# Performance work log

Measured on AMD Instinct MI355X. Metric: run time of the kernel, lower is better.

The kernel has to match this reference:

```python
import jax, jax.numpy as jnp
import numpy as np

N_QUBITS = 8

# Quantum circuit math: starting from |0...0>, apply RX(x_i) then RY(theta_i) on each
# wire independently (product state preserved). Exact PauliZ expectation per wire:
#   RX(x)|0> = cos(x/2)|0> - i sin(x/2)|1>;  after RY(t):
#   <Z> = cos(x) * cos(t)
# This is the exact closed form of the full state-vector simulation the torch module runs.

def setup_inputs() -> dict:
    key = jax.random.key(0)
    k1, k2, k3, k4 = jax.random.split(key, 4)
    B, S, D, F = 4, 4096, 1024, 4096
    x = jax.random.normal(k1, (B, S, D), dtype=jnp.float32)
    theta = jax.random.normal(k2, (N_QUBITS,), dtype=jnp.float32)
    W1 = jax.random.normal(k3, (F, N_QUBITS), dtype=jnp.float32) * (1.0 / np.sqrt(N_QUBITS))
    W2 = jax.random.normal(k4, (D, F), dtype=jnp.float32) * (1.0 / np.sqrt(F))
    return {"x": x, "theta": theta, "W1": W1, "W2": W2}


def reference(x, theta, W1, W2):
    # Encoder only reads the first n_qubits features of each token.
    z = jnp.cos(x[..., :N_QUBITS]) * jnp.cos(theta)          # [B, S, Q] PauliZ expectations
    h = jax.nn.relu(jnp.einsum('bsq,fq->bsf', z, W1))        # [B, S, ffn_dim]
    return jnp.einsum('bsf,df->bsd', h, W2)                  # [B, S, embed_dim]
```

## Files before the change

### kernel.cpp

```cpp
#include <hip/hip_runtime.h>
#include <hip/hip_bf16.h>
#include <math.h>


using f32x4  = __attribute__((ext_vector_type(4))) float;
using bf16x8 = __attribute__((ext_vector_type(8))) short;
using i32x4  = __attribute__((ext_vector_type(4))) int;

#define M_TOT 16384
#define N_TOT 1024
#define K_TOT 4096
#define NKT   128
#define TILEB 16384

static const size_t H_BYTES   = (size_t)M_TOT * K_TOT * 2;
static const size_t W2B_BYTES = (size_t)N_TOT * K_TOT * 2;
static const size_t WS_NEED   = H_BYTES + W2B_BYTES;

#define SWZ32(row, bytecol) ((bytecol) ^ ((((row) >> 1) & 3) << 4))

#define GLD16(gp, lp) __builtin_amdgcn_global_load_lds( \
    (const __attribute__((address_space(1))) unsigned int*)(const void*)(gp), \
    (__attribute__((address_space(3))) unsigned int*)(void*)(lp), 16, 0, 0)

static __device__ inline unsigned short f2bf(float f) {
    __hip_bfloat16 b = __float2bfloat16(f);
    unsigned short u;
    __builtin_memcpy(&u, &b, 2);
    return u;
}

__global__ __launch_bounds__(256)
void k_h(const float* __restrict__ x, const float* __restrict__ theta,
         const float* __restrict__ W1, char* __restrict__ hws)
{
    __shared__ float sZ[256 * 8];
    __shared__ float sW[128 * 8];
    const int tid = threadIdx.x;
    const int bx  = blockIdx.x;
    const int by  = blockIdx.y;

    {
        const float* xp = x + ((size_t)bx * 256 + tid) * 1024;
        f32x4 a = *reinterpret_cast<const f32x4*>(xp);
        f32x4 b = *reinterpret_cast<const f32x4*>(xp + 4);
        #pragma unroll
        for (int q = 0; q < 4; ++q) {
            sZ[tid * 8 + q]     = cosf(a[q]) * cosf(theta[q]);
            sZ[tid * 8 + 4 + q] = cosf(b[q]) * cosf(theta[q + 4]);
        }
    }
    *reinterpret_cast<f32x4*>(&sW[tid * 4]) =
        *reinterpret_cast<const f32x4*>(W1 + (size_t)by * 1024 + tid * 4);
    __syncthreads();

    const int tm = tid >> 4;
    const int tk = tid & 15;

    f32x4 wA[8], wB[8];
    #pragma unroll
    for (int kk = 0; kk < 8; ++kk) {
        wA[kk] = *reinterpret_cast<const f32x4*>(&sW[(tk * 8 + kk) * 8]);
        wB[kk] = *reinterpret_cast<const f32x4*>(&sW[(tk * 8 + kk) * 8 + 4]);
    }

    const int kt    = by * 4 + (tk >> 2);
    const int slotb = (tk & 3) * 16;
    char* tb = hws + ((size_t)bx * NKT + kt) * TILEB;

    #pragma unroll
    for (int i = 0; i < 16; ++i) {
        const int row = tm * 16 + i;
        f32x4 za = *reinterpret_cast<const f32x4*>(&sZ[row * 8]);
        f32x4 zb = *reinterpret_cast<const f32x4*>(&sZ[row * 8 + 4]);
        unsigned hu[8];
        #pragma unroll
        for (int kk = 0; kk < 8; ++kk) {
            float h = 0.f;
            #pragma unroll
            for (int q = 0; q < 4; ++q) {
                h = fmaf(za[q], wA[kk][q], h);
                h = fmaf(zb[q], wB[kk][q], h);
            }
            hu[kk] = (unsigned)f2bf(fmaxf(h, 0.f));
        }
        i32x4 pk;
        pk[0] = (int)(hu[0] | (hu[1] << 16));
        pk[1] = (int)(hu[2] | (hu[3] << 16));
        pk[2] = (int)(hu[4] | (hu[5] << 16));
        pk[3] = (int)(hu[6] | (hu[7] << 16));
        *reinterpret_cast<i32x4*>(tb + row * 64 + SWZ32(row, slotb)) = pk;
    }
}

__global__ __launch_bounds__(256)
void k_w2(const float* __restrict__ W2, char* __restrict__ w2ws)
{
    const int gt = blockIdx.x * 256 + threadIdx.x;
    const int n  = gt >> 9;
    const int k8 = gt & 511;
    const float* p = W2 + (size_t)n * K_TOT + k8 * 8;
    f32x4 a = *reinterpret_cast<const f32x4*>(p);
    f32x4 b = *reinterpret_cast<const f32x4*>(p + 4);
    i32x4 pk;
    pk[0] = (int)((unsigned)f2bf(a[0]) | ((unsigned)f2bf(a[1]) << 16));
    pk[1] = (int)((unsigned)f2bf(a[2]) | ((unsigned)f2bf(a[3]) << 16));
    pk[2] = (int)((unsigned)f2bf(b[0]) | ((unsigned)f2bf(b[1]) << 16));
    pk[3] = (int)((unsigned)f2bf(b[2]) | ((unsigned)f2bf(b[3]) << 16));
    const int nt = n >> 8, row = n & 255, kt = k8 >> 2, slotb = (k8 & 3) * 16;
    char* dst = w2ws + ((size_t)nt * NKT + kt) * TILEB + row * 64 + SWZ32(row, slotb);
    *reinterpret_cast<i32x4*>(dst) = pk;
}


#define KTILE_BODY(BUF, KT, DOSTAGE)                                              \
    bf16x8 a[4], a2[4], b[4];                                                     \
    _Pragma("unroll")                                                             \
    for (int i = 0; i < 4; ++i)                                                   \
        a[i] = *reinterpret_cast<const bf16x8*>(lds + (BUF) * 16384 + aoff[i]);   \
    _Pragma("unroll")                                                             \
    for (int j = 0; j < 4; ++j)                                                   \
        b[j] = *reinterpret_cast<const bf16x8*>(lds + 65536 + (BUF) * 16384 + boff[j]); \
    if (DOSTAGE) {                                                                \
        const char* g = aT + (size_t)((KT) + 3) * TILEB;                          \
        GLD16(g + tid * 16,        lds + (((BUF) + 3) & 3) * 16384 + wave * 1024);        \
        GLD16(g + 8192 + tid * 16, lds + (((BUF) + 3) & 3) * 16384 + 8192 + wave * 1024); \
    }                                                                             \
    __builtin_amdgcn_s_setprio(1);                                                \
    _Pragma("unroll")                                                             \
    for (int i = 0; i < 4; ++i)                                                   \
        _Pragma("unroll")                                                         \
        for (int j = 0; j < 4; ++j)                                               \
            acc[i][j] = __builtin_amdgcn_mfma_f32_16x16x32_bf16(a[i], b[j], acc[i][j], 0, 0, 0); \
    __builtin_amdgcn_s_setprio(0);                                                \
    _Pragma("unroll")                                                             \
    for (int i = 0; i < 4; ++i)                                                   \
        a2[i] = *reinterpret_cast<const bf16x8*>(lds + (BUF) * 16384 + aoff[i + 4]); \
    if (DOSTAGE) {                                                                \
        const char* g = bT + (size_t)((KT) + 3) * TILEB;                          \
        GLD16(g + tid * 16,        lds + 65536 + (((BUF) + 3) & 3) * 16384 + wave * 1024);        \
        GLD16(g + 8192 + tid * 16, lds + 65536 + (((BUF) + 3) & 3) * 16384 + 8192 + wave * 1024); \
    }                                                                             \
    __builtin_amdgcn_s_setprio(1);                                                \
    _Pragma("unroll")                                                             \
    for (int i = 0; i < 4; ++i)                                                   \
        _Pragma("unroll")                                                         \
        for (int j = 0; j < 4; ++j)                                               \
            acc[i + 4][j] = __builtin_amdgcn_mfma_f32_16x16x32_bf16(a2[i], b[j], acc[i + 4][j], 0, 0, 0); \
    __builtin_amdgcn_s_setprio(0);

#define KTILE(BUF, KT, DOSTAGE, WN) do {                                          \
    KTILE_BODY(BUF, KT, DOSTAGE)                                                  \
    asm volatile("s_waitcnt vmcnt(" #WN ")" ::: "memory");                        \
    __builtin_amdgcn_sched_barrier(0);                                            \
    __builtin_amdgcn_s_barrier();                                                 \
    __builtin_amdgcn_sched_barrier(0);                                            \
} while (0)

#define KTILE_LAST(BUF, KT) do { KTILE_BODY(BUF, KT, 0) } while (0)

__global__ __launch_bounds__(512, 2)
void k_gemm(const char* __restrict__ hws, const char* __restrict__ w2ws,
            float* __restrict__ out)
{
    __shared__ __align__(16) char lds[131072];

    const int tid  = threadIdx.x;
    const int lane = tid & 63;
    const int wave = tid >> 6;
    const int wm = wave >> 2;
    const int wn = wave & 3;
    const int mt = blockIdx.x;
    const int nt = blockIdx.y;

    const char* aT = hws  + (size_t)mt * NKT * TILEB;
    const char* bT = w2ws + (size_t)nt * NKT * TILEB;

    const int l16 = lane & 15;
    const int lkb = (lane >> 4) * 16;
    int aoff[8], boff[4];
    #pragma unroll
    for (int i = 0; i < 8; ++i) {
        const int row = wm * 128 + i * 16 + l16;
        aoff[i] = row * 64 + SWZ32(row, lkb);
    }
    #pragma unroll
    for (int j = 0; j < 4; ++j) {
        const int row = wn * 64 + j * 16 + l16;
        boff[j] = row * 64 + SWZ32(row, lkb);
    }

    f32x4 acc[8][4];
    #pragma unroll
    for (int i = 0; i < 8; ++i)
        #pragma unroll
        for (int j = 0; j < 4; ++j)
            acc[i][j] = {0.f, 0.f, 0.f, 0.f};

    #pragma unroll
    for (int t = 0; t < 3; ++t) {
        const char* ga = aT + (size_t)t * TILEB;
        const char* gb = bT + (size_t)t * TILEB;
        GLD16(ga + tid * 16,        lds + t * 16384 + wave * 1024);
        GLD16(ga + 8192 + tid * 16, lds + t * 16384 + 8192 + wave * 1024);
        GLD16(gb + tid * 16,        lds + 65536 + t * 16384 + wave * 1024);
        GLD16(gb + 8192 + tid * 16, lds + 65536 + t * 16384 + 8192 + wave * 1024);
    }
    asm volatile("s_waitcnt vmcnt(8)" ::: "memory");
    __builtin_amdgcn_sched_barrier(0);
    __builtin_amdgcn_s_barrier();
    __builtin_amdgcn_sched_barrier(0);

    #pragma unroll 1
    for (int t = 0; t < NKT - 4; t += 4) {
        KTILE(0, t,     1, 8);
        KTILE(1, t + 1, 1, 8);
        KTILE(2, t + 2, 1, 8);
        KTILE(3, t + 3, 1, 8);
    }
    KTILE(0, NKT - 4, 1, 8);
    KTILE(1, NKT - 3, 0, 4);
    KTILE(2, NKT - 2, 0, 0);
    KTILE_LAST(3, NKT - 1);

    const int orow0 = mt * 256 + wm * 128 + (lane >> 4) * 4;
    const int ocol0 = nt * 256 + wn * 64 + l16;
    #pragma unroll
    for (int i = 0; i < 8; ++i)
        #pragma unroll
        for (int j = 0; j < 4; ++j)
            #pragma unroll
            for (int jj = 0; jj < 4; ++jj)
                out[(size_t)(orow0 + i * 16 + jj) * N_TOT + (ocol0 + j * 16)] = acc[i][j][jj];
}

__global__ __launch_bounds__(256, 3)
void qffn_fused(const float* __restrict__ x, const float* __restrict__ theta,
                const float* __restrict__ W1, const float* __restrict__ W2,
                float* __restrict__ out)
{
    __shared__ __align__(16) unsigned short sA[128 * 64];
    __shared__ __align__(16) unsigned short sB[128 * 64];

    const int tid  = threadIdx.x;
    const int lane = tid & 63;
    const int wave = tid >> 6;
    const int m0 = blockIdx.x * 128;
    const int n0 = blockIdx.y * 128;

    const int arow = tid & 127;
    float zc[8];
    {
        const float* xp = x + (size_t)(m0 + arow) * 1024;
        f32x4 x0 = *reinterpret_cast<const f32x4*>(xp);
        f32x4 x1 = *reinterpret_cast<const f32x4*>(xp + 4);
        #pragma unroll
        for (int q = 0; q < 4; ++q) {
            zc[q]     = cosf(x0[q]) * cosf(theta[q]);
            zc[q + 4] = cosf(x1[q]) * cosf(theta[q + 4]);
        }
    }

    f32x4 acc[4][4];
    #pragma unroll
    for (int i = 0; i < 4; ++i)
        #pragma unroll
        for (int j = 0; j < 4; ++j)
            acc[i][j] = {0.f, 0.f, 0.f, 0.f};

    const int wr  = (wave >> 1) * 64;
    const int wc  = (wave & 1) * 64;
    const int l16 = lane & 15;
    const int lk8 = (lane >> 4) * 8;

    for (int k0 = 0; k0 < K_TOT; k0 += 64) {
        #pragma unroll
        for (int g = 0; g < 4; ++g) {
            const int cg  = (tid >> 7) + 2 * g;
            const int cgu = __builtin_amdgcn_readfirstlane(cg);
            const float* w1p = W1 + (size_t)(k0 + cgu * 8) * 8;
            i32x4 pk;
            #pragma unroll
            for (int p = 0; p < 4; ++p) {
                float h0 = 0.f, h1 = 0.f;
                #pragma unroll
                for (int q = 0; q < 8; ++q) {
                    h0 = fmaf(zc[q], w1p[(2 * p) * 8 + q], h0);
                    h1 = fmaf(zc[q], w1p[(2 * p + 1) * 8 + q], h1);
                }
                pk[p] = (int)(((unsigned)f2bf(fmaxf(h0, 0.f))) |
                              (((unsigned)f2bf(fmaxf(h1, 0.f))) << 16));
            }
            const int off = (arow * 64 + cg * 8) ^ ((arow & 7) << 3);
            *reinterpret_cast<i32x4*>(&sA[off]) = pk;
        }
        {
            const int fi = tid & 15;
            const int rb = tid >> 4;
            #pragma unroll
            for (int r = 0; r < 8; ++r) {
                const int row = rb + r * 16;
                f32x4 v = *(reinterpret_cast<const f32x4*>(W2 + (size_t)(n0 + row) * K_TOT + k0) + fi);
                unsigned p0 = (unsigned)f2bf(v[0]) | ((unsigned)f2bf(v[1]) << 16);
                unsigned p1 = (unsigned)f2bf(v[2]) | ((unsigned)f2bf(v[3]) << 16);
                const int off = (row * 64 + fi * 4) ^ ((row & 7) << 3);
                *reinterpret_cast<unsigned*>(&sB[off])     = p0;
                *reinterpret_cast<unsigned*>(&sB[off + 2]) = p1;
            }
        }
        __syncthreads();

        #pragma unroll
        for (int s = 0; s < 2; ++s) {
            bf16x8 af[4], bfr[4];
            #pragma unroll
            for (int i = 0; i < 4; ++i) {
                const int row = wr + i * 16 + l16;
                const int off = (row * 64 + s * 32 + lk8) ^ ((row & 7) << 3);
                af[i] = *reinterpret_cast<const bf16x8*>(&sA[off]);
            }
            #pragma unroll
            for (int j = 0; j < 4; ++j) {
                const int row = wc + j * 16 + l16;
                const int off = (row * 64 + s * 32 + lk8) ^ ((row & 7) << 3);
                bfr[j] = *reinterpret_cast<const bf16x8*>(&sB[off]);
            }
            #pragma unroll
            for (int i = 0; i < 4; ++i)
                #pragma unroll
                for (int j = 0; j < 4; ++j)
                    acc[i][j] = __builtin_amdgcn_mfma_f32_16x16x32_bf16(af[i], bfr[j], acc[i][j], 0, 0, 0);
        }
        __syncthreads();
    }

    const int orow0 = m0 + wr + (lane >> 4) * 4;
    const int ocol0 = n0 + wc + l16;
    #pragma unroll
    for (int i = 0; i < 4; ++i)
        #pragma unroll
        for (int j = 0; j < 4; ++j)
            #pragma unroll
            for (int jj = 0; jj < 4; ++jj)
                out[(size_t)(orow0 + i * 16 + jj) * N_TOT + (ocol0 + j * 16)] = acc[i][j][jj];
}

extern "C" void kernel_launch(void* const* d_in, const int* in_sizes, int n_in,
                              void* d_out, int out_size, void* d_ws, size_t ws_size,
                              hipStream_t stream) {
    const float* x     = (const float*)d_in[0];
    const float* theta = (const float*)d_in[1];
    const float* W1    = (const float*)d_in[2];
    const float* W2    = (const float*)d_in[3];
    float* out = (float*)d_out;

    if (ws_size >= WS_NEED) {
        char* hws  = (char*)d_ws;
        char* w2ws = (char*)d_ws + H_BYTES;

        k_h<<<dim3(M_TOT / 256, K_TOT / 128), dim3(256), 0, stream>>>(x, theta, W1, hws);
        k_w2<<<dim3((N_TOT * K_TOT / 8) / 256), dim3(256), 0, stream>>>(W2, w2ws);
        k_gemm<<<dim3(M_TOT / 256, N_TOT / 256), dim3(512), 0, stream>>>(hws, w2ws, out);
    } else {
        qffn_fused<<<dim3(M_TOT / 128, N_TOT / 128), dim3(256), 0, stream>>>(x, theta, W1, W2, out);
    }
}
```

Baseline: 146.2 us.

## Merge prep kernels and software-pipeline LDS fragment reads in GEMM loop

Fuses the hidden-activation kernel and the W2 bf16 conversion kernel into one launch, with the block index selecting the role, so one kernel launch and its tail gap go away. The GEMM main loop is restructured so that LDS fragments for the next k-tile are read into a second register set while MFMAs run on the current set, with a single barrier per phase and all four global-to-LDS stages issued together. This aims to hide LDS read latency behind matrix math. It doubles the fragment register footprint and changes the vmcnt waits, which may raise register pressure at 2 blocks per CU.

```diff
diff --git a/kernel.cpp b/kernel.cpp
--- a/kernel.cpp
+++ b/kernel.cpp
@@ -31,139 +31,136 @@
 }
 
 __global__ __launch_bounds__(256)
-void k_h(const float* __restrict__ x, const float* __restrict__ theta,
-         const float* __restrict__ W1, char* __restrict__ hws)
+void k_prep(const float* __restrict__ x, const float* __restrict__ theta,
+            const float* __restrict__ W1, const float* __restrict__ W2,
+            char* __restrict__ hws, char* __restrict__ w2ws)
 {
     __shared__ float sZ[256 * 8];
     __shared__ float sW[128 * 8];
     const int tid = threadIdx.x;
-    const int bx  = blockIdx.x;
-    const int by  = blockIdx.y;
-
-    {
-        const float* xp = x + ((size_t)bx * 256 + tid) * 1024;
-        f32x4 a = *reinterpret_cast<const f32x4*>(xp);
-        f32x4 b = *reinterpret_cast<const f32x4*>(xp + 4);
-        #pragma unroll
-        for (int q = 0; q < 4; ++q) {
-            sZ[tid * 8 + q]     = cosf(a[q]) * cosf(theta[q]);
-            sZ[tid * 8 + 4 + q] = cosf(b[q]) * cosf(theta[q + 4]);
-        }
-    }
-    *reinterpret_cast<f32x4*>(&sW[tid * 4]) =
-        *reinterpret_cast<const f32x4*>(W1 + (size_t)by * 1024 + tid * 4);
-    __syncthreads();
-
-    const int tm = tid >> 4;
-    const int tk = tid & 15;
-
-    f32x4 wA[8], wB[8];
-    #pragma unroll
-    for (int kk = 0; kk < 8; ++kk) {
-        wA[kk] = *reinterpret_cast<const f32x4*>(&sW[(tk * 8 + kk) * 8]);
-        wB[kk] = *reinterpret_cast<const f32x4*>(&sW[(tk * 8 + kk) * 8 + 4]);
-    }
-
-    const int kt    = by * 4 + (tk >> 2);
-    const int slotb = (tk & 3) * 16;
-    char* tb = hws + ((size_t)bx * NKT + kt) * TILEB;
-
-    #pragma unroll
-    for (int i = 0; i < 16; ++i) {
-        const int row = tm * 16 + i;
-        f32x4 za = *reinterpret_cast<const f32x4*>(&sZ[row * 8]);
-        f32x4 zb = *reinterpret_cast<const f32x4*>(&sZ[row * 8 + 4]);
-        unsigned hu[8];
+
+    if (blockIdx.x < 2048) {
+        const int bx = blockIdx.x >> 5;
+        const int by = blockIdx.x & 31;
+
+        {
+            const float* xp = x + ((size_t)bx * 256 + tid) * 1024;
+            f32x4 a = *reinterpret_cast<const f32x4*>(xp);
+            f32x4 b = *reinterpret_cast<const f32x4*>(xp + 4);
+            #pragma unroll
+            for (int q = 0; q < 4; ++q) {
+                sZ[tid * 8 + q]     = cosf(a[q]) * cosf(theta[q]);
+                sZ[tid * 8 + 4 + q] = cosf(b[q]) * cosf(theta[q + 4]);
+            }
+        }
+        *reinterpret_cast<f32x4*>(&sW[tid * 4]) =
+            *reinterpret_cast<const f32x4*>(W1 + (size_t)by * 1024 + tid * 4);
+        __syncthreads();
+
+        const int tm = tid >> 4;
+        const int tk = tid & 15;
+
+        f32x4 wA[8], wB[8];
         #pragma unroll
         for (int kk = 0; kk < 8; ++kk) {
-            float h = 0.f;
-            #pragma unroll
-            for (int q = 0; q < 4; ++q) {
-                h = fmaf(za[q], wA[kk][q], h);
-                h = fmaf(zb[q], wB[kk][q], h);
-            }
-            hu[kk] = (unsigned)f2bf(fmaxf(h, 0.f));
-        }
+            wA[kk] = *reinterpret_cast<const f32x4*>(&sW[(tk * 8 + kk) * 8]);
+            wB[kk] = *reinterpret_cast<const f32x4*>(&sW[(tk * 8 + kk) * 8 + 4]);
+        }
+
+        const int kt    = by * 4 + (tk >> 2);
+        const int slotb = (tk & 3) * 16;
+        char* tb = hws + ((size_t)bx * NKT + kt) * TILEB;
+
+        #pragma unroll
+        for (int i = 0; i < 16; ++i) {
+            const int row = tm * 16 + i;
+            f32x4 za = *reinterpret_cast<const f32x4*>(&sZ[row * 8]);
+            f32x4 zb = *reinterpret_cast<const f32x4*>(&sZ[row * 8 + 4]);
+            unsigned hu[8];
+            #pragma unroll
+            for (int kk = 0; kk < 8; ++kk) {
+                float h = 0.f;
+                #pragma unroll
+                for (int q = 0; q < 4; ++q) {
+                    h = fmaf(za[q], wA[kk][q], h);
+                    h = fmaf(zb[q], wB[kk][q], h);
+                }
+                hu[kk] = (unsigned)f2bf(fmaxf(h, 0.f));
+            }
+            i32x4 pk;
+            pk[0] = (int)(hu[0] | (hu[1] << 16));
+            pk[1] = (int)(hu[2] | (hu[3] << 16));
+            pk[2] = (int)(hu[4] | (hu[5] << 16));
+            pk[3] = (int)(hu[6] | (hu[7] << 16));
+            *reinterpret_cast<i32x4*>(tb + row * 64 + SWZ32(row, slotb)) = pk;
+        }
+    } else {
+        const int gt = (blockIdx.x - 2048) * 256 + tid;
+        const int n  = gt >> 9;
+        const int k8 = gt & 511;
+        const float* p = W2 + (size_t)n * K_TOT + k8 * 8;
+        f32x4 a = *reinterpret_cast<const f32x4*>(p);
+        f32x4 b = *reinterpret_cast<const f32x4*>(p + 4);
         i32x4 pk;
-        pk[0] = (int)(hu[0] | (hu[1] << 16));
-        pk[1] = (int)(hu[2] | (hu[3] << 16));
-        pk[2] = (int)(hu[4] | (hu[5] << 16));
-        pk[3] = (int)(hu[6] | (hu[7] << 16));
-        *reinterpret_cast<i32x4*>(tb + row * 64 + SWZ32(row, slotb)) = pk;
-    }
-}
-
-__global__ __launch_bounds__(256)
-void k_w2(const float* __restrict__ W2, char* __restrict__ w2ws)
-{
-    const int gt = blockIdx.x * 256 + threadIdx.x;
-    const int n  = gt >> 9;
-    const int k8 = gt & 511;
-    const float* p = W2 + (size_t)n * K_TOT + k8 * 8;
-    f32x4 a = *reinterpret_cast<const f32x4*>(p);
-    f32x4 b = *reinterpret_cast<const f32x4*>(p + 4);
-    i32x4 pk;
-    pk[0] = (int)((unsigned)f2bf(a[0]) | ((unsigned)f2bf(a[1]) << 16));
-    pk[1] = (int)((unsigned)f2bf(a[2]) | ((unsigned)f2bf(a[3]) << 16));
-    pk[2] = (int)((unsigned)f2bf(b[0]) | ((unsigned)f2bf(b[1]) << 16));
-    pk[3] = (int)((unsigned)f2bf(b[2]) | ((unsigned)f2bf(b[3]) << 16));
-    const int nt = n >> 8, row = n & 255, kt = k8 >> 2, slotb = (k8 & 3) * 16;
-    char* dst = w2ws + ((size_t)nt * NKT + kt) * TILEB + row * 64 + SWZ32(row, slotb);
-    *reinterpret_cast<i32x4*>(dst) = pk;
-}
-
-
-#define KTILE_BODY(BUF, KT, DOSTAGE)                                              \
-    bf16x8 a[4], a2[4], b[4];                                                     \
+        pk[0] = (int)((unsigned)f2bf(a[0]) | ((unsigned)f2bf(a[1]) << 16));
+        pk[1] = (int)((unsigned)f2bf(a[2]) | ((unsigned)f2bf(a[3]) << 16));
+        pk[2] = (int)((unsigned)f2bf(b[0]) | ((unsigned)f2bf(b[1]) << 16));
+        pk[3] = (int)((unsigned)f2bf(b[2]) | ((unsigned)f2bf(b[3]) << 16));
+        const int nt = n >> 8, row = n & 255, kt = k8 >> 2, slotb = (k8 & 3) * 16;
+        char* dst = w2ws + ((size_t)nt * NKT + kt) * TILEB + row * 64 + SWZ32(row, slotb);
+        *reinterpret_cast<i32x4*>(dst) = pk;
+    }
+}
+
+
+#define DS_FRAGS(RD, BUF1) do {                                                   \
+    const char* sa_ = ldsA + (BUF1) * 16384;                                      \
+    const char* sb_ = ldsB + (BUF1) * 16384;                                      \
     _Pragma("unroll")                                                             \
-    for (int i = 0; i < 4; ++i)                                                   \
-        a[i] = *reinterpret_cast<const bf16x8*>(lds + (BUF) * 16384 + aoff[i]);   \
+    for (int i = 0; i < 8; ++i)                                                   \
+        Pa[RD][i] = *reinterpret_cast<const bf16x8*>(sa_ + aoff + i * 1024);      \
     _Pragma("unroll")                                                             \
     for (int j = 0; j < 4; ++j)                                                   \
-        b[j] = *reinterpret_cast<const bf16x8*>(lds + 65536 + (BUF) * 16384 + boff[j]); \
-    if (DOSTAGE) {                                                                \
-        const char* g = aT + (size_t)((KT) + 3) * TILEB;                          \
-        GLD16(g + tid * 16,        lds + (((BUF) + 3) & 3) * 16384 + wave * 1024);        \
-        GLD16(g + 8192 + tid * 16, lds + (((BUF) + 3) & 3) * 16384 + 8192 + wave * 1024); \
-    }                                                                             \
+        Pb[RD][j] = *reinterpret_cast<const bf16x8*>(sb_ + boff + j * 1024);      \
+} while (0)
+
+#define STAGE4(KT3, BUF3) do {                                                    \
+    const char* ga_ = aT + (size_t)(KT3) * TILEB;                                 \
+    const char* gb_ = bT + (size_t)(KT3) * TILEB;                                 \
+    GLD16(ga_ + gofs,        ldsA + (BUF3) * 16384 + lofs);                       \
+    GLD16(ga_ + 8192 + gofs, ldsA + (BUF3) * 16384 + 8192 + lofs);                \
+    GLD16(gb_ + gofs,        ldsB + (BUF3) * 16384 + lofs);                       \
+    GLD16(gb_ + 8192 + gofs, ldsB + (BUF3) * 16384 + 8192 + lofs);                \
+} while (0)
+
+#define MFMA32(USE) do {                                                          \
     __builtin_amdgcn_s_setprio(1);                                                \
     _Pragma("unroll")                                                             \
-    for (int i = 0; i < 4; ++i)                                                   \
+    for (int i = 0; i < 8; ++i)                                                   \
         _Pragma("unroll")                                                         \
         for (int j = 0; j < 4; ++j)                                               \
-            acc[i][j] = __builtin_amdgcn_mfma_f32_16x16x32_bf16(a[i], b[j], acc[i][j], 0, 0, 0); \
+            acc[i][j] = __builtin_amdgcn_mfma_f32_16x16x32_bf16(Pa[USE][i], Pb[USE][j], acc[i][j], 0, 0, 0); \
     __builtin_amdgcn_s_setprio(0);                                                \
-    _Pragma("unroll")                                                             \
-    for (int i = 0; i < 4; ++i)                                                   \
-        a2[i] = *reinterpret_cast<const bf16x8*>(lds + (BUF) * 16384 + aoff[i + 4]); \
-    if (DOSTAGE) {                                                                \
-        const char* g = bT + (size_t)((KT) + 3) * TILEB;                          \
-        GLD16(g + tid * 16,        lds + 65536 + (((BUF) + 3) & 3) * 16384 + wave * 1024);        \
-        GLD16(g + 8192 + tid * 16, lds + 65536 + (((BUF) + 3) & 3) * 16384 + 8192 + wave * 1024); \
-    }                                                                             \
-    __builtin_amdgcn_s_setprio(1);                                                \
-    _Pragma("unroll")                                                             \
-    for (int i = 0; i < 4; ++i)                                                   \
-        _Pragma("unroll")                                                         \
-        for (int j = 0; j < 4; ++j)                                               \
-            acc[i + 4][j] = __builtin_amdgcn_mfma_f32_16x16x32_bf16(a2[i], b[j], acc[i + 4][j], 0, 0, 0); \
-    __builtin_amdgcn_s_setprio(0);
-
-#define KTILE(BUF, KT, DOSTAGE, WN) do {                                          \
-    KTILE_BODY(BUF, KT, DOSTAGE)                                                  \
+} while (0)
+
+#define PHASE(BUF, KT, WN, DOREAD, DOSTAGE) do {                                  \
     asm volatile("s_waitcnt vmcnt(" #WN ")" ::: "memory");                        \
     __builtin_amdgcn_sched_barrier(0);                                            \
     __builtin_amdgcn_s_barrier();                                                 \
     __builtin_amdgcn_sched_barrier(0);                                            \
+    if (DOREAD)  DS_FRAGS(((BUF) + 1) & 1, ((BUF) + 1) & 3);                      \
+    if (DOSTAGE) STAGE4((KT) + 3, ((BUF) + 3) & 3);                               \
+    __builtin_amdgcn_sched_barrier(0);                                            \
+    MFMA32((BUF) & 1);                                                            \
 } while (0)
-
-#define KTILE_LAST(BUF, KT) do { KTILE_BODY(BUF, KT, 0) } while (0)
 
 __global__ __launch_bounds__(512, 2)
 void k_gemm(const char* __restrict__ hws, const char* __restrict__ w2ws,
             float* __restrict__ out)
 {
     __shared__ __align__(16) char lds[131072];
+    char* const ldsA = lds;
+    char* const ldsB = lds + 65536;
 
     const int tid  = threadIdx.x;
     const int lane = tid & 63;
@@ -178,17 +175,16 @@
 
     const int l16 = lane & 15;
     const int lkb = (lane >> 4) * 16;
-    int aoff[8], boff[4];
-    #pragma unroll
-    for (int i = 0; i < 8; ++i) {
-        const int row = wm * 128 + i * 16 + l16;
-        aoff[i] = row * 64 + SWZ32(row, lkb);
-    }
-    #pragma unroll
-    for (int j = 0; j < 4; ++j) {
-        const int row = wn * 64 + j * 16 + l16;
-        boff[j] = row * 64 + SWZ32(row, lkb);
-    }
+    const int arow0 = wm * 128 + l16;
+    const int aoff  = arow0 * 64 + SWZ32(arow0, lkb);
+    const int brow0 = wn * 64 + l16;
+    const int boff  = brow0 * 64 + SWZ32(brow0, lkb);
+
+    const int gofs = tid * 16;
+    const int lofs = wave * 1024;
+
+    bf16x8 Pa[2][8];
+    bf16x8 Pb[2][4];
 
     f32x4 acc[8][4];
     #pragma unroll
@@ -197,31 +193,26 @@
         for (int j = 0; j < 4; ++j)
             acc[i][j] = {0.f, 0.f, 0.f, 0.f};
 
-    #pragma unroll
-    for (int t = 0; t < 3; ++t) {
-        const char* ga = aT + (size_t)t * TILEB;
-        const char* gb = bT + (size_t)t * TILEB;
-        GLD16(ga + tid * 16,        lds + t * 16384 + wave * 1024);
-        GLD16(ga + 8192 + tid * 16, lds + t * 16384 + 8192 + wave * 1024);
-        GLD16(gb + tid * 16,        lds + 65536 + t * 16384 + wave * 1024);
-        GLD16(gb + 8192 + tid * 16, lds + 65536 + t * 16384 + 8192 + wave * 1024);
-    }
+    STAGE4(0, 0);
+    STAGE4(1, 1);
+    STAGE4(2, 2);
     asm volatile("s_waitcnt vmcnt(8)" ::: "memory");
     __builtin_amdgcn_sched_barrier(0);
     __builtin_amdgcn_s_barrier();
     __builtin_amdgcn_sched_barrier(0);
+    DS_FRAGS(0, 0);
 
     #pragma unroll 1
-    for (int t = 0; t < NKT - 4; t += 4) {
-        KTILE(0, t,     1, 8);
-        KTILE(1, t + 1, 1, 8);
-        KTILE(2, t + 2, 1, 8);
-        KTILE(3, t + 3, 1, 8);
-    }
-    KTILE(0, NKT - 4, 1, 8);
-    KTILE(1, NKT - 3, 0, 4);
-    KTILE(2, NKT - 2, 0, 0);
-    KTILE_LAST(3, NKT - 1);
+    for (int t = 0; t < 124; t += 4) {
+        PHASE(0, t,     4, 1, 1);
+        PHASE(1, t + 1, 4, 1, 1);
+        PHASE(2, t + 2, 4, 1, 1);
+        PHASE(3, t + 3, 4, 1, 1);
+    }
+    PHASE(0, 124, 4, 1, 1);
+    PHASE(1, 125, 4, 1, 0);
+    PHASE(2, 126, 0, 1, 0);
+    MFMA32(1);
 
     const int orow0 = mt * 256 + wm * 128 + (lane >> 4) * 4;
     const int ocol0 = nt * 256 + wn * 64 + l16;
@@ -358,8 +349,7 @@
         char* hws  = (char*)d_ws;
         char* w2ws = (char*)d_ws + H_BYTES;
 
-        k_h<<<dim3(M_TOT / 256, K_TOT / 128), dim3(256), 0, stream>>>(x, theta, W1, hws);
-        k_w2<<<dim3((N_TOT * K_TOT / 8) / 256), dim3(256), 0, stream>>>(W2, w2ws);
+        k_prep<<<dim3(4096), dim3(256), 0, stream>>>(x, theta, W1, W2, hws, w2ws);
         k_gemm<<<dim3(M_TOT / 256, N_TOT / 256), dim3(512), 0, stream>>>(hws, w2ws, out);
     } else {
         qffn_fused<<<dim3(M_TOT / 128, N_TOT / 128), dim3(256), 0, stream>>>(x, theta, W1, W2, out);
```

Measured after the change: 146.5 us. Within noise of the previous version (+0.1%).
